# Optimization experiments

Measured on AMD Instinct MI355X. Metric: run time of the kernel, lower is better.

The kernel has to match this reference:

```python
import jax, jax.numpy as jnp
import numpy as np

SHORT = 2000
CUTVALS = [0, 2000, 12000, 40000, 100000]  # [0] + cutoffs + [n_classes]
OSZ = [10000, 28000, 60000]
HSZ = [384, 192, 96]
IN_F = 768
LN_EPS = 1e-5


def setup_inputs() -> dict:
    key = jax.random.key(0)
    ks = jax.random.split(key, 16)
    B, L = 256, 20
    inp = {
        "x": jax.random.normal(ks[0], (B, IN_F), jnp.float32),
        "head_W": jax.random.normal(ks[1], (SHORT + 3, IN_F), jnp.float32) / np.sqrt(IN_F),
        "target": jax.random.randint(ks[2], (B, L), 0, CUTVALS[-1], jnp.int64)
        if jax.config.jax_enable_x64 else jax.random.randint(ks[2], (B, L), 0, CUTVALS[-1], jnp.int32),
    }
    for i in range(3):
        inp[f"w1_{i}"] = jax.random.normal(ks[3 + 4 * i], (HSZ[i], IN_F), jnp.float32) / np.sqrt(IN_F)
        inp[f"g{i}"] = jnp.ones((HSZ[i],), jnp.float32)
        inp[f"b{i}"] = jnp.zeros((HSZ[i],), jnp.float32)
        inp[f"w2_{i}"] = jax.random.normal(ks[4 + 4 * i], (OSZ[i], HSZ[i]), jnp.float32) / np.sqrt(HSZ[i])
    return inp


def _bce_with_logits(logits, y):
    # matches torch BCEWithLogitsLoss(reduction='none')
    return jnp.maximum(logits, 0.0) - logits * y + jnp.log1p(jnp.exp(-jnp.abs(logits)))


def reference(x, head_W, w1_0, g0, b0, w2_0, w1_1, g1, b1, w2_1, w1_2, g2, b2, w2_2, target):
    W1, G, Bp, W2 = [w1_0, w1_1, w1_2], [g0, g1, g2], [b0, b1, b2], [w2_0, w2_1, w2_2]
    B = x.shape[0]
    rows = jnp.arange(B)[:, None]
    dt = x.dtype

    head_logits = x @ head_W.T  # [B, SHORT + n_clusters]

    # shortlist multi-hot (rows with no shortlist label stay all-zero, as in torch)
    m0 = target < SHORT
    onehot_short = jnp.zeros((B, SHORT), dt).at[rows, jnp.clip(target, 0, SHORT - 1)].max(m0.astype(dt))

    total_cluster = jnp.zeros((B,), dt)
    actives = []
    for i in range(3):
        low, high = CUTVALS[i + 1], CUTVALS[i + 2]
        osz = high - low
        m = (target >= low) & (target < high)  # [B, L]
        active = m.any(axis=1).astype(dt)      # [B]
        actives.append(active)
        # multi-hot targets for this cluster
        y = jnp.zeros((B, osz), dt).at[rows, jnp.clip(target - low, 0, osz - 1)].max(m.astype(dt))
        # tail projection: Linear -> LayerNorm -> ReLU -> Linear
        h = x @ W1[i].T
        mu = h.mean(-1, keepdims=True)
        var = ((h - mu) ** 2).mean(-1, keepdims=True)
        h = jax.nn.relu((h - mu) * jax.lax.rsqrt(var + LN_EPS) * G[i] + Bp[i])
        # p = sigmoid(cluster-root logit) * sigmoid(tail logits)
        root = jax.nn.sigmoid(head_logits[:, SHORT + i])[:, None]  # [B,1]
        p = root * jax.nn.sigmoid(h @ W2[i].T)                     # [B, osz]
        # torch BCELoss clamps log at -100
        bce = -(y * jnp.maximum(jnp.log(p), -100.0) + (1.0 - y) * jnp.maximum(jnp.log1p(-p), -100.0))
        total_cluster = total_cluster + active * bce.sum(axis=1)

    cluster_onehot = jnp.stack(actives, axis=1)  # [B, 3]
    head_y = jnp.concatenate([onehot_short, cluster_onehot], axis=1)
    head_loss = _bce_with_logits(head_logits, head_y)  # [B, SHORT+3]
    mult = (cluster_onehot == 0).astype(dt)
    head_loss = jnp.concatenate([head_loss[:, :SHORT], head_loss[:, SHORT:] * mult], axis=1)
    head_loss = head_loss.sum(axis=1)

    csz = jnp.asarray(OSZ, dt)
    num_loss = (mult + cluster_onehot * csz).sum(axis=1) + SHORT
    return ((head_loss + total_cluster) / num_loss).mean()
```

## Files before the change

kernel.cpp:

```cpp
#include <hip/hip_runtime.h>
#include <hip/hip_bf16.h>

#define INF 768
#define NSHORT 2000
#define NHEAD 2003

typedef __attribute__((ext_vector_type(8))) short  s16x8;
typedef __attribute__((ext_vector_type(4))) float  f32x4;
typedef __attribute__((ext_vector_type(8))) float  f32x8;

__device__ __forceinline__ float sigf(float z) { return 1.f / (1.f + __expf(-z)); }
__device__ __forceinline__ float softplusf(float z) {
    return fmaxf(z, 0.f) + __logf(1.f + __expf(-fabsf(z)));
}
__device__ __forceinline__ float qreduce16(float v) {
    v += __shfl_xor(v, 1); v += __shfl_xor(v, 2);
    v += __shfl_xor(v, 4); v += __shfl_xor(v, 8);
    return v;
}
__device__ __forceinline__ float wreduce64(float v) {
    v += __shfl_xor(v, 1);  v += __shfl_xor(v, 2);  v += __shfl_xor(v, 4);
    v += __shfl_xor(v, 8);  v += __shfl_xor(v, 16); v += __shfl_xor(v, 32);
    return v;
}
__device__ __forceinline__ short bfc(float x) {
    union { __hip_bfloat16 h; short s; } u; u.h = __float2bfloat16(x); return u.s;
}

template <int K32>
__device__ __forceinline__ void perm_B(const float* __restrict__ W, int N,
                                       __hip_bfloat16* __restrict__ dst, int c) {
    const int lane = c & 63, t2 = c >> 6;
    const int ct = t2 & 3, t3 = t2 >> 2;
    const int j = t3 % K32, stripe = t3 / K32;
    int col = stripe * 64 + ct * 16 + (lane & 15);
    if (col >= N) col = N - 1;
    const int k0 = j * 32 + (lane >> 4) * 8;
    const f32x8 v = *(const f32x8*)(W + (size_t)col * (K32 * 32) + k0);
    s16x8 o;
#pragma unroll
    for (int i = 0; i < 8; i++) o[i] = bfc(v[i]);
    *(s16x8*)((short*)dst + (size_t)c * 8) = o;
}
template <int K32>
__device__ __forceinline__ void perm_A(const float* __restrict__ X,
                                       __hip_bfloat16* __restrict__ dst, int c) {
    const int lane = c & 63, t2 = c >> 6;
    const int j = t2 % K32, rt = t2 / K32;
    const int row = rt * 16 + (lane & 15);
    const int k0 = j * 32 + (lane >> 4) * 8;
    const f32x8 v = *(const f32x8*)(X + (size_t)row * (K32 * 32) + k0);
    s16x8 o;
#pragma unroll
    for (int i = 0; i < 8; i++) o[i] = bfc(v[i]);
    *(s16x8*)((short*)dst + (size_t)c * 8) = o;
}

template <int K32, int RT, int MODE>
__device__ __forceinline__ void core_p(
    const __hip_bfloat16* __restrict__ Ap,
    const __hip_bfloat16* __restrict__ Wp, int N,
    int stripe, int rtb0, int j0, int kstr,
    float* __restrict__ outH, int ldH,
    float* __restrict__ part, int pslot,
    const float* __restrict__ rootlogit, int ci)
{
    const int t = threadIdx.x;
    const int wave = t >> 6, lane = t & 63;
    const int quad = lane >> 4, l16 = lane & 15;
    const int rtb = rtb0 + wave * RT;

    const short* ap[RT];
#pragma unroll
    for (int rt = 0; rt < RT; rt++)
        ap[rt] = (const short*)Ap + (((size_t)(rtb + rt) * kstr + j0) * 64 + lane) * 8;
    const short* wp[4];
#pragma unroll
    for (int ct = 0; ct < 4; ct++)
        wp[ct] = (const short*)Wp + ((((size_t)stripe * kstr + j0) * 4 + ct) * 64 + lane) * 8;

    s16x8 af[2][RT], wf[2][4];
#pragma unroll
    for (int rt = 0; rt < RT; rt++) af[0][rt] = *(const s16x8*)(ap[rt]);
#pragma unroll
    for (int ct = 0; ct < 4; ct++) wf[0][ct] = *(const s16x8*)(wp[ct]);

    f32x4 acc[RT][4];
#pragma unroll
    for (int rt = 0; rt < RT; rt++)
#pragma unroll
        for (int ct = 0; ct < 4; ct++) acc[rt][ct] = (f32x4){0.f, 0.f, 0.f, 0.f};

#pragma unroll
    for (int j = 0; j < K32; j++) {
        const int b = j & 1, nb = b ^ 1;
        if (j + 1 < K32) {
#pragma unroll
            for (int rt = 0; rt < RT; rt++)
                af[nb][rt] = *(const s16x8*)(ap[rt] + (size_t)(j + 1) * 512);
#pragma unroll
            for (int ct = 0; ct < 4; ct++)
                wf[nb][ct] = *(const s16x8*)(wp[ct] + (size_t)(j + 1) * 2048);
        }
#pragma unroll
        for (int rt = 0; rt < RT; rt++)
#pragma unroll
            for (int ct = 0; ct < 4; ct++)
                acc[rt][ct] = __builtin_amdgcn_mfma_f32_16x16x32_bf16(
                    af[b][rt], wf[b][ct], acc[rt][ct], 0, 0, 0);
    }

    const int col0 = stripe * 64;
    if (MODE == 0) {
#pragma unroll
        for (int rt = 0; rt < RT; rt++)
#pragma unroll
            for (int ct = 0; ct < 4; ct++) {
                const int col = col0 + ct * 16 + l16;
                if (col < N) {
#pragma unroll
                    for (int r = 0; r < 4; r++)
                        outH[(size_t)((rtb + rt) * 16 + quad * 4 + r) * ldH + col] =
                            acc[rt][ct][r];
                }
            }
    } else {
#pragma unroll
        for (int rt = 0; rt < RT; rt++) {
#pragma unroll
            for (int r = 0; r < 4; r++) {
                const int row = (rtb + rt) * 16 + quad * 4 + r;
                const float rv = sigf(rootlogit[row * 3 + ci]);
                float pd = 1.f, pn = 1.f;
#pragma unroll
                for (int ct = 0; ct < 4; ct++) {
                    const int col = col0 + ct * 16 + l16;
                    const float tv = fminf(__expf(-acc[rt][ct][r]), 1e6f);
                    const float d = (col < N) ? (1.f + tv) : 1.f;
                    const float n = (col < N) ? (1.f + tv - rv) : 1.f;
                    pd *= d; pn *= n;
                }
                float s = __logf(pd) - __logf(pn);
                s = qreduce16(s);
                if (l16 == 0) part[(size_t)pslot * 256 + row] = s;
            }
        }
    }
}

__global__ __launch_bounds__(256) void k_pre(
    const float* __restrict__ x, const float* __restrict__ headW,
    const float* __restrict__ w10, const float* __restrict__ w11, const float* __restrict__ w12,
    const float* __restrict__ w20, const float* __restrict__ w21, const float* __restrict__ w22,
    __hip_bfloat16* xbp, __hip_bfloat16* hWp,
    __hip_bfloat16* w10p, __hip_bfloat16* w11p, __hip_bfloat16* w12p,
    __hip_bfloat16* w20p, __hip_bfloat16* w21p, __hip_bfloat16* w22p,
    float* __restrict__ rootlogit) {
    const int bx = blockIdx.x, t = threadIdx.x;
    if (bx < 256) {
        const int row = bx, wave = t >> 6, lane = t & 63;
        if (wave < 3) {
            const float* xr = x + row * INF;
            const float* wr = headW + (size_t)(NSHORT + wave) * INF;
            float s = 0.f;
            for (int k = lane; k < INF; k += 64) s += xr[k] * wr[k];
            s = wreduce64(s);
            if (lane == 0) rootlogit[row * 3 + wave] = s;
        }
    } else if (bx < 352)  perm_A<24>(x, xbp, (bx - 256) * 256 + t);
    else if (bx < 1120) perm_B<24>(headW, NHEAD, hWp, (bx - 352) * 256 + t);
    else if (bx < 1264) perm_B<24>(w10, 384, w10p, (bx - 1120) * 256 + t);
    else if (bx < 1336) perm_B<24>(w11, 192, w11p, (bx - 1264) * 256 + t);
    else if (bx < 1384) perm_B<24>(w12, 96, w12p, (bx - 1336) * 256 + t);
    else if (bx < 3268) perm_B<12>(w20, 10000, w20p, (bx - 1384) * 256 + t);
    else if (bx < 5896) perm_B<6>(w21, 28000, w21p, (bx - 3268) * 256 + t);
    else                perm_B<3>(w22, 60000, w22p, (bx - 5896) * 256 + t);
}

__global__ __launch_bounds__(256, 4) void k_mm1(const __hip_bfloat16* __restrict__ xbp,
                                                const __hip_bfloat16* hWp,
                                                const __hip_bfloat16* w10p,
                                                const __hip_bfloat16* w11p,
                                                const __hip_bfloat16* w12p,
                                                float* zA, float* zB,
                                                float* h0a, float* h0b,
                                                float* h1a, float* h1b,
                                                float* h2a, float* h2b) {
    const int bx = blockIdx.x;
    if (bx < 128) {
        const int kq = bx & 1, rg = (bx >> 1) & 1, stripe = bx >> 2;
        core_p<12, 2, 0>(xbp, hWp, NHEAD, stripe, rg * 8, kq * 12, 24,
                         kq ? zB : zA, 2048, nullptr, 0, nullptr, 0);
    } else if (bx < 152) {
        const int m = bx - 128, stripe = m >> 2, rg = (m >> 1) & 1, kq = m & 1;
        core_p<12, 2, 0>(xbp, w10p, 384, stripe, rg * 8, kq * 12, 24,
                         kq ? h0b : h0a, 384, nullptr, 0, nullptr, 0);
    } else if (bx < 164) {
        const int m = bx - 152, stripe = m >> 2, rg = (m >> 1) & 1, kq = m & 1;
        core_p<12, 2, 0>(xbp, w11p, 192, stripe, rg * 8, kq * 12, 24,
                         kq ? h1b : h1a, 192, nullptr, 0, nullptr, 0);
    } else {
        const int m = bx - 164, stripe = m >> 2, rg = (m >> 1) & 1, kq = m & 1;
        core_p<12, 2, 0>(xbp, w12p, 96, stripe, rg * 8, kq * 12, 24,
                         kq ? h2b : h2a, 96, nullptr, 0, nullptr, 0);
    }
}

__global__ __launch_bounds__(256) void k_ln(const float* h0a, const float* h0b,
                                            const float* h1a, const float* h1b,
                                            const float* h2a, const float* h2b,
                                            const float* g0, const float* g1, const float* g2,
                                            const float* b0, const float* b1, const float* b2,
                                            const float* zA, const float* zB,
                                            __hip_bfloat16* f0, __hip_bfloat16* f1,
                                            __hip_bfloat16* f2,
                                            __hip_bfloat16* p0, __hip_bfloat16* p1,
                                            __hip_bfloat16* p2,
                                            float* __restrict__ phead) {
    const int bx = blockIdx.x;
    if (bx < 192) {
        const int task = bx * 4 + (threadIdx.x >> 6);
        const int ci = task >> 8, row = task & 255, lane = threadIdx.x & 63;
        const float *ha, *hb, *g, *bb; __hip_bfloat16 *fo, *po; int hsz, K32;
        if (ci == 0)      { ha = h0a; hb = h0b; g = g0; bb = b0; fo = f0; po = p0; hsz = 384; K32 = 12; }
        else if (ci == 1) { ha = h1a; hb = h1b; g = g1; bb = b1; fo = f1; po = p1; hsz = 192; K32 = 6; }
        else              { ha = h2a; hb = h2b; g = g2; bb = b2; fo = f2; po = p2; hsz = 96;  K32 = 3; }
        const float* hra = ha + row * hsz;
        const float* hrb = hb + row * hsz;
        float s = 0.f, s2 = 0.f;
        for (int k = lane; k < hsz; k += 64) {
            const float v = hra[k] + hrb[k]; s += v; s2 += v * v;
        }
        s = wreduce64(s); s2 = wreduce64(s2);
        const float mu = s / hsz;
        const float var = s2 / hsz - mu * mu;
        const float rsn = rsqrtf(var + 1e-5f);
        const int nch = hsz >> 3;
        if (lane < nch) {
            const f32x8 va = *(const f32x8*)(hra + lane * 8);
            const f32x8 vb = *(const f32x8*)(hrb + lane * 8);
            const f32x8 gg = *(const f32x8*)(g + lane * 8);
            const f32x8 bv = *(const f32x8*)(bb + lane * 8);
            s16x8 o;
#pragma unroll
            for (int i = 0; i < 8; i++)
                o[i] = bfc(fmaxf((va[i] + vb[i] - mu) * rsn * gg[i] + bv[i], 0.f));
            *(s16x8*)((short*)fo + (size_t)row * hsz + lane * 8) = o;
            const size_t chunk = ((size_t)(row >> 4) * K32 + (lane >> 2)) * 64
                               + (lane & 3) * 16 + (row & 15);
            *(s16x8*)((short*)po + chunk * 8) = o;
        }
    } else {
        const int row = bx - 192, t = threadIdx.x;
        const int wave = t >> 6, lane = t & 63;
        float val = 0.f;
        if (t < 250) {
            const f32x8 a = *(const f32x8*)(zA + (size_t)row * 2048 + t * 8);
            const f32x8 b = *(const f32x8*)(zB + (size_t)row * 2048 + t * 8);
            float m = 0.f, P = 1.f;
#pragma unroll
            for (int i = 0; i < 8; i++) {
                const float z = a[i] + b[i];
                m += fmaxf(z, 0.f);
                P *= 1.f + __expf(-fabsf(z));
            }
            val = m + __logf(P);
        }
        val = wreduce64(val);
        __shared__ float red[4];
        if (lane == 0) red[wave] = val;
        __syncthreads();
        if (t == 0) phead[row] = red[0] + red[1] + red[2] + red[3];
    }
}

__global__ __launch_bounds__(256, 4) void k_bce(const __hip_bfloat16* p0,
                                                const __hip_bfloat16* p1,
                                                const __hip_bfloat16* p2,
                                                const __hip_bfloat16* w20p,
                                                const __hip_bfloat16* w21p,
                                                const __hip_bfloat16* w22p,
                                                float* __restrict__ part,
                                                const float* __restrict__ rootlogit) {
    const int bx = blockIdx.x;
    const int s = bx >> 1, rg = bx & 1;
    if (s < 157)
        core_p<12, 2, 2>(p0, w20p, 10000, s, rg * 8, 0, 12,
                         nullptr, 0, part, s, rootlogit, 0);
    else if (s < 595)
        core_p<6, 2, 2>(p1, w21p, 28000, s - 157, rg * 8, 0, 6,
                        nullptr, 0, part, s, rootlogit, 1);
    else
        core_p<3, 2, 2>(p2, w22p, 60000, s - 595, rg * 8, 0, 3,
                        nullptr, 0, part, s, rootlogit, 2);
}

__global__ __launch_bounds__(256) void k_red(const float* __restrict__ part,
                                             const float* __restrict__ phead,
                                             const float* __restrict__ rootlogit,
                                             const int* __restrict__ target,
                                             const float* __restrict__ x,
                                             const float* __restrict__ headW,
                                             const __hip_bfloat16* f0,
                                             const __hip_bfloat16* f1,
                                             const __hip_bfloat16* f2,
                                             const float* w20, const float* w21, const float* w22,
                                             float* __restrict__ out) {
    const int row = blockIdx.x;
    const int t = threadIdx.x, wave = t >> 6, lane = t & 63;
    __shared__ float sx[INF];
    __shared__ __hip_bfloat16 shb[384 + 192 + 96];
    __shared__ int st[20];
    __shared__ float scorr[4];
    __shared__ float red[4][4];
    for (int i = t; i < INF; i += 256) sx[i] = x[row * INF + i];
    for (int i = t; i < 384; i += 256) shb[i] = f0[row * 384 + i];
    for (int i = t; i < 192; i += 256) shb[384 + i] = f1[row * 192 + i];
    for (int i = t; i < 96; i += 256)  shb[576 + i] = f2[row * 96 + i];
    if (t < 20) st[t] = target[row * 20 + t];
    if (t < 4) scorr[t] = 0.f;
    __syncthreads();
    for (int l = wave; l < 20; l += 4) {
        const int tg = st[l];
        bool dup = false;
        for (int m = 0; m < l; m++) dup |= (st[m] == tg);
        if (dup) continue;
        if (tg < NSHORT) {
            const float* wr = headW + (size_t)tg * INF;
            float z = 0.f;
            for (int k = lane; k < INF; k += 64) z += sx[k] * wr[k];
            z = wreduce64(z);
            if (lane == 0) atomicAdd(&scorr[3], -z);
        } else {
            int ci, low, hsz, hoff; const float* w2;
            if (tg < 12000)      { ci = 0; low = 2000;  hsz = 384; hoff = 0;   w2 = w20; }
            else if (tg < 40000) { ci = 1; low = 12000; hsz = 192; hoff = 384; w2 = w21; }
            else                 { ci = 2; low = 40000; hsz = 96;  hoff = 576; w2 = w22; }
            const float* wr = w2 + (size_t)(tg - low) * hsz;
            float z = 0.f;
            for (int k = lane; k < hsz; k += 64)
                z += __bfloat162float(shb[hoff + k]) * wr[k];
            z = wreduce64(z);
            if (lane == 0) {
                const float rvv = sigf(rootlogit[row * 3 + ci]);
                const float p = rvv * sigf(z);
                atomicAdd(&scorr[ci],
                          -fmaxf(__logf(p), -100.f) + fmaxf(__logf(1.f - p), -100.f));
            }
        }
    }
    float c0 = 0.f, c1 = 0.f, c2 = 0.f;
    for (int i = t; i < 1533; i += 256) {
        const float v = part[(size_t)i * 256 + row];
        if (i < 157) c0 += v; else if (i < 595) c1 += v; else c2 += v;
    }
    c0 = wreduce64(c0); c1 = wreduce64(c1); c2 = wreduce64(c2);
    if (lane == 0) { red[0][wave] = c0; red[1][wave] = c1; red[2][wave] = c2; }
    __syncthreads();
    if (t == 0) {
        float cc[3];
        for (int i = 0; i < 3; i++) cc[i] = red[i][0] + red[i][1] + red[i][2] + red[i][3];
        float hsum = phead[row] + scorr[3];
        bool act[3] = {false, false, false};
        for (int l = 0; l < 20; l++) {
            const int tg = target[row * 20 + l];
            if (tg >= 2000) {
                if (tg < 12000) act[0] = true;
                else if (tg < 40000) act[1] = true;
                else act[2] = true;
            }
        }
        float total = 0.f, num = 2000.f;
        const float csz[3] = {10000.f, 28000.f, 60000.f};
        for (int i = 0; i < 3; i++) {
            if (act[i]) { total += cc[i] + scorr[i]; num += csz[i]; }
            else        { hsum += softplusf(rootlogit[row * 3 + i]); num += 1.f; }
        }
        atomicAdd(out, (hsum + total) / num * (1.f / 256.f));
    }
}

extern "C" void kernel_launch(void* const* d_in, const int* in_sizes, int n_in,
                              void* d_out, int out_size, void* d_ws, size_t ws_size,
                              hipStream_t stream) {
    const float* x      = (const float*)d_in[0];
    const float* headW  = (const float*)d_in[1];
    const int*   target = (const int*)d_in[2];
    const float* w10 = (const float*)d_in[3];
    const float* g0  = (const float*)d_in[4];
    const float* b0  = (const float*)d_in[5];
    const float* w20 = (const float*)d_in[6];
    const float* w11 = (const float*)d_in[7];
    const float* g1  = (const float*)d_in[8];
    const float* b1  = (const float*)d_in[9];
    const float* w21 = (const float*)d_in[10];
    const float* w12 = (const float*)d_in[11];
    const float* g2  = (const float*)d_in[12];
    const float* b2  = (const float*)d_in[13];
    const float* w22 = (const float*)d_in[14];
    float* out = (float*)d_out;

    char* ws = (char*)d_ws;
    size_t off = 0;
    auto carve = [&](size_t bytes) -> void* {
        void* p = ws + off;
        off += (bytes + 255) & ~(size_t)255;
        return p;
    };
    __hip_bfloat16* xbp  = (__hip_bfloat16*)carve((size_t)256 * 768 * 2);
    __hip_bfloat16* hWp  = (__hip_bfloat16*)carve((size_t)2048 * 768 * 2);
    __hip_bfloat16* w10p = (__hip_bfloat16*)carve((size_t)384 * 768 * 2);
    __hip_bfloat16* w11p = (__hip_bfloat16*)carve((size_t)192 * 768 * 2);
    __hip_bfloat16* w12p = (__hip_bfloat16*)carve((size_t)128 * 768 * 2);
    __hip_bfloat16* w20p = (__hip_bfloat16*)carve((size_t)10048 * 384 * 2);
    __hip_bfloat16* w21p = (__hip_bfloat16*)carve((size_t)28032 * 192 * 2);
    __hip_bfloat16* w22p = (__hip_bfloat16*)carve((size_t)60032 * 96 * 2);
    float* zA            = (float*)carve((size_t)256 * 2048 * 4);
    float* zB            = (float*)carve((size_t)256 * 2048 * 4);
    float* h0a           = (float*)carve((size_t)256 * 384 * 4);
    float* h0b           = (float*)carve((size_t)256 * 384 * 4);
    float* h1a           = (float*)carve((size_t)256 * 192 * 4);
    float* h1b           = (float*)carve((size_t)256 * 192 * 4);
    float* h2a           = (float*)carve((size_t)256 * 96 * 4);
    float* h2b           = (float*)carve((size_t)256 * 96 * 4);
    __hip_bfloat16* f0   = (__hip_bfloat16*)carve((size_t)256 * 384 * 2);
    __hip_bfloat16* f1   = (__hip_bfloat16*)carve((size_t)256 * 192 * 2);
    __hip_bfloat16* f2   = (__hip_bfloat16*)carve((size_t)256 * 96 * 2);
    __hip_bfloat16* p0   = (__hip_bfloat16*)carve((size_t)256 * 384 * 2);
    __hip_bfloat16* p1   = (__hip_bfloat16*)carve((size_t)256 * 192 * 2);
    __hip_bfloat16* p2   = (__hip_bfloat16*)carve((size_t)256 * 96 * 2);
    float* rootlogit     = (float*)carve((size_t)256 * 3 * 4);
    float* phead         = (float*)carve((size_t)256 * 4);
    float* part          = (float*)carve((size_t)1536 * 256 * 4);

    hipMemsetAsync(out, 0, sizeof(float), stream);

    k_pre<<<8710, 256, 0, stream>>>(x, headW, w10, w11, w12, w20, w21, w22,
                                    xbp, hWp, w10p, w11p, w12p, w20p, w21p, w22p,
                                    rootlogit);
    k_mm1<<<172, 256, 0, stream>>>(xbp, hWp, w10p, w11p, w12p,
                                   zA, zB, h0a, h0b, h1a, h1b, h2a, h2b);
    k_ln<<<448, 256, 0, stream>>>(h0a, h0b, h1a, h1b, h2a, h2b,
                                  g0, g1, g2, b0, b1, b2, zA, zB,
                                  f0, f1, f2, p0, p1, p2, phead);
    k_bce<<<3066, 256, 0, stream>>>(p0, p1, p2, w20p, w21p, w22p, part, rootlogit);
    k_red<<<256, 256, 0, stream>>>(part, phead, rootlogit, target, x, headW,
                                   f0, f1, f2, w20, w21, w22, out);

    (void)in_sizes; (void)n_in; (void)out_size; (void)ws_size;
}
```

Baseline: 186.1 us.

## Fuse weight bf16 conversion into GEMM blocks via LDS staging, drop pre-permute kernel

Removes the separate k_pre kernel, which converted and permuted every fp32 weight matrix to a bf16 fragment layout in a global workspace. Each GEMM block now loads its 64-column stripe of fp32 weights straight from the inputs, converts it to bf16 into shared memory, and reads the MFMA fragments from LDS. Each block covers all 256 rows, so the block count is halved. The first GEMM also converts the fp32 activations x on the fly. This avoids writing and re-reading the permuted weight copies and one kernel launch. In exchange, the fp32 weights are read at full width inside the GEMM kernels, which use more LDS and have lower occupancy (launch bounds 3).

```diff
diff --git a/kernel.cpp b/kernel.cpp
--- a/kernel.cpp
+++ b/kernel.cpp
@@ -27,40 +27,11 @@
     union { __hip_bfloat16 h; short s; } u; u.h = __float2bfloat16(x); return u.s;
 }
 
-template <int K32>
-__device__ __forceinline__ void perm_B(const float* __restrict__ W, int N,
-                                       __hip_bfloat16* __restrict__ dst, int c) {
-    const int lane = c & 63, t2 = c >> 6;
-    const int ct = t2 & 3, t3 = t2 >> 2;
-    const int j = t3 % K32, stripe = t3 / K32;
-    int col = stripe * 64 + ct * 16 + (lane & 15);
-    if (col >= N) col = N - 1;
-    const int k0 = j * 32 + (lane >> 4) * 8;
-    const f32x8 v = *(const f32x8*)(W + (size_t)col * (K32 * 32) + k0);
-    s16x8 o;
-#pragma unroll
-    for (int i = 0; i < 8; i++) o[i] = bfc(v[i]);
-    *(s16x8*)((short*)dst + (size_t)c * 8) = o;
-}
-template <int K32>
-__device__ __forceinline__ void perm_A(const float* __restrict__ X,
-                                       __hip_bfloat16* __restrict__ dst, int c) {
-    const int lane = c & 63, t2 = c >> 6;
-    const int j = t2 % K32, rt = t2 / K32;
-    const int row = rt * 16 + (lane & 15);
-    const int k0 = j * 32 + (lane >> 4) * 8;
-    const f32x8 v = *(const f32x8*)(X + (size_t)row * (K32 * 32) + k0);
-    s16x8 o;
-#pragma unroll
-    for (int i = 0; i < 8; i++) o[i] = bfc(v[i]);
-    *(s16x8*)((short*)dst + (size_t)c * 8) = o;
-}
-
-template <int K32, int RT, int MODE>
-__device__ __forceinline__ void core_p(
-    const __hip_bfloat16* __restrict__ Ap,
-    const __hip_bfloat16* __restrict__ Wp, int N,
-    int stripe, int rtb0, int j0, int kstr,
+template <int K32, int MODE, int AF32>
+__device__ __forceinline__ void core_s(
+    const void* __restrict__ Av, int ldA, int kbase,
+    const float* __restrict__ W, int Kfull, int N, int stripe,
+    short* __restrict__ lds,
     float* __restrict__ outH, int ldH,
     float* __restrict__ part, int pslot,
     const float* __restrict__ rootlogit, int ci)
@@ -68,26 +39,54 @@
     const int t = threadIdx.x;
     const int wave = t >> 6, lane = t & 63;
     const int quad = lane >> 4, l16 = lane & 15;
-    const int rtb = rtb0 + wave * RT;
-
-    const short* ap[RT];
-#pragma unroll
-    for (int rt = 0; rt < RT; rt++)
-        ap[rt] = (const short*)Ap + (((size_t)(rtb + rt) * kstr + j0) * 64 + lane) * 8;
-    const short* wp[4];
+    const int rtb = wave * 4;
+
+    {
+        const int ct = t >> 6, l = t & 63;
+        int col = stripe * 64 + ct * 16 + (l & 15);
+        if (col >= N) col = N - 1;
+        const float* src = W + (size_t)col * Kfull + kbase + (l >> 4) * 8;
+        short* dst = lds + ((size_t)ct * 64 + l) * 8;
+#pragma unroll
+        for (int s = 0; s < K32; s++) {
+            const f32x8 v = *(const f32x8*)(src + s * 32);
+            s16x8 o;
+#pragma unroll
+            for (int i = 0; i < 8; i++) o[i] = bfc(v[i]);
+            *(s16x8*)(dst + (size_t)s * 2048) = o;
+        }
+    }
+
+    s16x8 af[2][4];
+    const float* axp[4];
+    const short* app[4];
+    if (AF32) {
+#pragma unroll
+        for (int rt = 0; rt < 4; rt++) {
+            axp[rt] = (const float*)Av + (size_t)((rtb + rt) * 16 + l16) * ldA + kbase + quad * 8;
+            const f32x8 v = *(const f32x8*)(axp[rt]);
+#pragma unroll
+            for (int i = 0; i < 8; i++) af[0][rt][i] = bfc(v[i]);
+        }
+    } else {
+#pragma unroll
+        for (int rt = 0; rt < 4; rt++) {
+            app[rt] = (const short*)Av + ((size_t)(rtb + rt) * ldA * 64 + lane) * 8;
+            af[0][rt] = *(const s16x8*)(app[rt]);
+        }
+    }
+
+    __syncthreads();
+
+    const short* wbase = lds + (size_t)lane * 8;
+    s16x8 wf[2][4];
 #pragma unroll
     for (int ct = 0; ct < 4; ct++)
-        wp[ct] = (const short*)Wp + ((((size_t)stripe * kstr + j0) * 4 + ct) * 64 + lane) * 8;
-
-    s16x8 af[2][RT], wf[2][4];
-#pragma unroll
-    for (int rt = 0; rt < RT; rt++) af[0][rt] = *(const s16x8*)(ap[rt]);
-#pragma unroll
-    for (int ct = 0; ct < 4; ct++) wf[0][ct] = *(const s16x8*)(wp[ct]);
-
-    f32x4 acc[RT][4];
-#pragma unroll
-    for (int rt = 0; rt < RT; rt++)
+        wf[0][ct] = *(const s16x8*)(wbase + (size_t)ct * 512);
+
+    f32x4 acc[4][4];
+#pragma unroll
+    for (int rt = 0; rt < 4; rt++)
 #pragma unroll
         for (int ct = 0; ct < 4; ct++) acc[rt][ct] = (f32x4){0.f, 0.f, 0.f, 0.f};
 
@@ -95,15 +94,24 @@
     for (int j = 0; j < K32; j++) {
         const int b = j & 1, nb = b ^ 1;
         if (j + 1 < K32) {
-#pragma unroll
-            for (int rt = 0; rt < RT; rt++)
-                af[nb][rt] = *(const s16x8*)(ap[rt] + (size_t)(j + 1) * 512);
+            if (AF32) {
+#pragma unroll
+                for (int rt = 0; rt < 4; rt++) {
+                    const f32x8 v = *(const f32x8*)(axp[rt] + (size_t)(j + 1) * 32);
+#pragma unroll
+                    for (int i = 0; i < 8; i++) af[nb][rt][i] = bfc(v[i]);
+                }
+            } else {
+#pragma unroll
+                for (int rt = 0; rt < 4; rt++)
+                    af[nb][rt] = *(const s16x8*)(app[rt] + (size_t)(j + 1) * 512);
+            }
 #pragma unroll
             for (int ct = 0; ct < 4; ct++)
-                wf[nb][ct] = *(const s16x8*)(wp[ct] + (size_t)(j + 1) * 2048);
-        }
-#pragma unroll
-        for (int rt = 0; rt < RT; rt++)
+                wf[nb][ct] = *(const s16x8*)(wbase + (size_t)(j + 1) * 2048 + ct * 512);
+        }
+#pragma unroll
+        for (int rt = 0; rt < 4; rt++)
 #pragma unroll
             for (int ct = 0; ct < 4; ct++)
                 acc[rt][ct] = __builtin_amdgcn_mfma_f32_16x16x32_bf16(
@@ -113,7 +121,7 @@
     const int col0 = stripe * 64;
     if (MODE == 0) {
 #pragma unroll
-        for (int rt = 0; rt < RT; rt++)
+        for (int rt = 0; rt < 4; rt++)
 #pragma unroll
             for (int ct = 0; ct < 4; ct++) {
                 const int col = col0 + ct * 16 + l16;
@@ -126,7 +134,7 @@
             }
     } else {
 #pragma unroll
-        for (int rt = 0; rt < RT; rt++) {
+        for (int rt = 0; rt < 4; rt++) {
 #pragma unroll
             for (int r = 0; r < 4; r++) {
                 const int row = (rtb + rt) * 16 + quad * 4 + r;
@@ -148,17 +156,34 @@
     }
 }
 
-__global__ __launch_bounds__(256) void k_pre(
+__global__ __launch_bounds__(256, 3) void k_mm1(
     const float* __restrict__ x, const float* __restrict__ headW,
-    const float* __restrict__ w10, const float* __restrict__ w11, const float* __restrict__ w12,
-    const float* __restrict__ w20, const float* __restrict__ w21, const float* __restrict__ w22,
-    __hip_bfloat16* xbp, __hip_bfloat16* hWp,
-    __hip_bfloat16* w10p, __hip_bfloat16* w11p, __hip_bfloat16* w12p,
-    __hip_bfloat16* w20p, __hip_bfloat16* w21p, __hip_bfloat16* w22p,
-    float* __restrict__ rootlogit) {
-    const int bx = blockIdx.x, t = threadIdx.x;
-    if (bx < 256) {
-        const int row = bx, wave = t >> 6, lane = t & 63;
+    const float* __restrict__ w10, const float* __restrict__ w11,
+    const float* __restrict__ w12,
+    float* zA, float* zB,
+    float* h0a, float* h0b, float* h1a, float* h1b, float* h2a, float* h2b,
+    float* __restrict__ rootlogit)
+{
+    __shared__ __align__(16) short smem[64 * 12 * 32];
+    const int bx = blockIdx.x;
+    if (bx < 64) {
+        const int stripe = bx >> 1, kq = bx & 1;
+        core_s<12, 0, 1>(x, INF, kq * 384, headW, INF, NHEAD, stripe, smem,
+                         kq ? zB : zA, 2048, nullptr, 0, nullptr, 0);
+    } else if (bx < 76) {
+        const int m = bx - 64, stripe = m >> 1, kq = m & 1;
+        core_s<12, 0, 1>(x, INF, kq * 384, w10, INF, 384, stripe, smem,
+                         kq ? h0b : h0a, 384, nullptr, 0, nullptr, 0);
+    } else if (bx < 82) {
+        const int m = bx - 76, stripe = m >> 1, kq = m & 1;
+        core_s<12, 0, 1>(x, INF, kq * 384, w11, INF, 192, stripe, smem,
+                         kq ? h1b : h1a, 192, nullptr, 0, nullptr, 0);
+    } else if (bx < 86) {
+        const int m = bx - 82, stripe = m >> 1, kq = m & 1;
+        core_s<12, 0, 1>(x, INF, kq * 384, w12, INF, 96, stripe, smem,
+                         kq ? h2b : h2a, 96, nullptr, 0, nullptr, 0);
+    } else {
+        const int row = bx - 86, wave = threadIdx.x >> 6, lane = threadIdx.x & 63;
         if (wave < 3) {
             const float* xr = x + row * INF;
             const float* wr = headW + (size_t)(NSHORT + wave) * INF;
@@ -167,42 +192,6 @@
             s = wreduce64(s);
             if (lane == 0) rootlogit[row * 3 + wave] = s;
         }
-    } else if (bx < 352)  perm_A<24>(x, xbp, (bx - 256) * 256 + t);
-    else if (bx < 1120) perm_B<24>(headW, NHEAD, hWp, (bx - 352) * 256 + t);
-    else if (bx < 1264) perm_B<24>(w10, 384, w10p, (bx - 1120) * 256 + t);
-    else if (bx < 1336) perm_B<24>(w11, 192, w11p, (bx - 1264) * 256 + t);
-    else if (bx < 1384) perm_B<24>(w12, 96, w12p, (bx - 1336) * 256 + t);
-    else if (bx < 3268) perm_B<12>(w20, 10000, w20p, (bx - 1384) * 256 + t);
-    else if (bx < 5896) perm_B<6>(w21, 28000, w21p, (bx - 3268) * 256 + t);
-    else                perm_B<3>(w22, 60000, w22p, (bx - 5896) * 256 + t);
-}
-
-__global__ __launch_bounds__(256, 4) void k_mm1(const __hip_bfloat16* __restrict__ xbp,
-                                                const __hip_bfloat16* hWp,
-                                                const __hip_bfloat16* w10p,
-                                                const __hip_bfloat16* w11p,
-                                                const __hip_bfloat16* w12p,
-                                                float* zA, float* zB,
-                                                float* h0a, float* h0b,
-                                                float* h1a, float* h1b,
-                                                float* h2a, float* h2b) {
-    const int bx = blockIdx.x;
-    if (bx < 128) {
-        const int kq = bx & 1, rg = (bx >> 1) & 1, stripe = bx >> 2;
-        core_p<12, 2, 0>(xbp, hWp, NHEAD, stripe, rg * 8, kq * 12, 24,
-                         kq ? zB : zA, 2048, nullptr, 0, nullptr, 0);
-    } else if (bx < 152) {
-        const int m = bx - 128, stripe = m >> 2, rg = (m >> 1) & 1, kq = m & 1;
-        core_p<12, 2, 0>(xbp, w10p, 384, stripe, rg * 8, kq * 12, 24,
-                         kq ? h0b : h0a, 384, nullptr, 0, nullptr, 0);
-    } else if (bx < 164) {
-        const int m = bx - 152, stripe = m >> 2, rg = (m >> 1) & 1, kq = m & 1;
-        core_p<12, 2, 0>(xbp, w11p, 192, stripe, rg * 8, kq * 12, 24,
-                         kq ? h1b : h1a, 192, nullptr, 0, nullptr, 0);
-    } else {
-        const int m = bx - 164, stripe = m >> 2, rg = (m >> 1) & 1, kq = m & 1;
-        core_p<12, 2, 0>(xbp, w12p, 96, stripe, rg * 8, kq * 12, 24,
-                         kq ? h2b : h2a, 96, nullptr, 0, nullptr, 0);
     }
 }
 
@@ -274,24 +263,24 @@
     }
 }
 
-__global__ __launch_bounds__(256, 4) void k_bce(const __hip_bfloat16* p0,
+__global__ __launch_bounds__(256, 3) void k_bce(const __hip_bfloat16* p0,
                                                 const __hip_bfloat16* p1,
                                                 const __hip_bfloat16* p2,
-                                                const __hip_bfloat16* w20p,
-                                                const __hip_bfloat16* w21p,
-                                                const __hip_bfloat16* w22p,
+                                                const float* __restrict__ w20,
+                                                const float* __restrict__ w21,
+                                                const float* __restrict__ w22,
                                                 float* __restrict__ part,
                                                 const float* __restrict__ rootlogit) {
-    const int bx = blockIdx.x;
-    const int s = bx >> 1, rg = bx & 1;
+    __shared__ __align__(16) short smem[64 * 12 * 32];
+    const int s = blockIdx.x;
     if (s < 157)
-        core_p<12, 2, 2>(p0, w20p, 10000, s, rg * 8, 0, 12,
+        core_s<12, 2, 0>(p0, 12, 0, w20, 384, 10000, s, smem,
                          nullptr, 0, part, s, rootlogit, 0);
     else if (s < 595)
-        core_p<6, 2, 2>(p1, w21p, 28000, s - 157, rg * 8, 0, 6,
+        core_s<6, 2, 0>(p1, 6, 0, w21, 192, 28000, s - 157, smem,
                         nullptr, 0, part, s, rootlogit, 1);
     else
-        core_p<3, 2, 2>(p2, w22p, 60000, s - 595, rg * 8, 0, 3,
+        core_s<3, 2, 0>(p2, 3, 0, w22, 96, 60000, s - 595, smem,
                         nullptr, 0, part, s, rootlogit, 2);
 }
 
@@ -407,14 +396,6 @@
         off += (bytes + 255) & ~(size_t)255;
         return p;
     };
-    __hip_bfloat16* xbp  = (__hip_bfloat16*)carve((size_t)256 * 768 * 2);
-    __hip_bfloat16* hWp  = (__hip_bfloat16*)carve((size_t)2048 * 768 * 2);
-    __hip_bfloat16* w10p = (__hip_bfloat16*)carve((size_t)384 * 768 * 2);
-    __hip_bfloat16* w11p = (__hip_bfloat16*)carve((size_t)192 * 768 * 2);
-    __hip_bfloat16* w12p = (__hip_bfloat16*)carve((size_t)128 * 768 * 2);
-    __hip_bfloat16* w20p = (__hip_bfloat16*)carve((size_t)10048 * 384 * 2);
-    __hip_bfloat16* w21p = (__hip_bfloat16*)carve((size_t)28032 * 192 * 2);
-    __hip_bfloat16* w22p = (__hip_bfloat16*)carve((size_t)60032 * 96 * 2);
     float* zA            = (float*)carve((size_t)256 * 2048 * 4);
     float* zB            = (float*)carve((size_t)256 * 2048 * 4);
     float* h0a           = (float*)carve((size_t)256 * 384 * 4);
@@ -435,15 +416,12 @@
 
     hipMemsetAsync(out, 0, sizeof(float), stream);
 
-    k_pre<<<8710, 256, 0, stream>>>(x, headW, w10, w11, w12, w20, w21, w22,
-                                    xbp, hWp, w10p, w11p, w12p, w20p, w21p, w22p,
-                                    rootlogit);
-    k_mm1<<<172, 256, 0, stream>>>(xbp, hWp, w10p, w11p, w12p,
-                                   zA, zB, h0a, h0b, h1a, h1b, h2a, h2b);
+    k_mm1<<<342, 256, 0, stream>>>(x, headW, w10, w11, w12,
+                                   zA, zB, h0a, h0b, h1a, h1b, h2a, h2b, rootlogit);
     k_ln<<<448, 256, 0, stream>>>(h0a, h0b, h1a, h1b, h2a, h2b,
                                   g0, g1, g2, b0, b1, b2, zA, zB,
                                   f0, f1, f2, p0, p1, p2, phead);
-    k_bce<<<3066, 256, 0, stream>>>(p0, p1, p2, w20p, w21p, w22p, part, rootlogit);
+    k_bce<<<1533, 256, 0, stream>>>(p0, p1, p2, w20, w21, w22, part, rootlogit);
     k_red<<<256, 256, 0, stream>>>(part, phead, rootlogit, target, x, headW,
                                    f0, f1, f2, w20, w21, w22, out);
 
```

After: 187.5 us. Within noise of the previous version (+0.7%).
